# Kernel tuning notes

Hardware: AMD Instinct MI355X
Metric: run time of the kernel (lower is better)

Reference implementation:

```python
import jax, jax.numpy as jnp
import numpy as np

SEQ, IN, H = 8192, 1024, 2048

def setup_inputs() -> dict:
    key = jax.random.key(0)
    ks = jax.random.split(key, 7)
    s = 0.02
    return {
        "input_seq": jax.random.normal(ks[0], (SEQ, IN), jnp.float32),
        "W_ih": jax.random.normal(ks[1], (4 * H, IN), jnp.float32) * s,
        "W_hh": jax.random.normal(ks[2], (4 * H, H), jnp.float32) * s,
        "b_ih": jax.random.normal(ks[3], (4 * H,), jnp.float32) * s,
        "b_hh": jax.random.normal(ks[4], (4 * H,), jnpp if False else jnp.float32) * s if False else jax.random.normal(ks[4], (4 * H,), jnp.float32) * s,
        "W_lin": jax.random.normal(ks[5], (1, H), jnp.float32) * s,
        "b_lin": jax.random.normal(ks[6], (1,), jnp.float32) * s,
    }

def _lstm(input_seq, W_ih, W_hh, b, H):
    # Precompute input projections for all timesteps: [S, 4H]
    x_proj = input_seq @ W_ih.T + b

    def step(carry, xp):
        h, c = carry
        gates = xp + h @ W_hh.T  # [4H], PyTorch order: i, f, g, o
        i = jax.nn.sigmoid(gates[0:H])
        f = jax.nn.sigmoid(gates[H:2 * H])
        g = jnp.tanh(gates[2 * H:3 * H])
        o = jax.nn.sigmoid(gates[3 * H:4 * H])
        c = f * c + i * g
        h = o * jnp.tanh(c)
        return (h, c), h

    h0 = jnp.zeros((H,), input_seq.dtype)
    c0 = jnp.zeros((H,), input_seq.dtype)
    _, hs = jax.lax.scan(step, (h0, c0), x_proj)
    return hs  # [S, H]

def reference(input_seq, W_ih, W_hh, b_ih, b_hh, W_lin, b_lin):
    H_ = W_hh.shape[1]
    hs = _lstm(input_seq, W_ih, W_hh, b_ih + b_hh, H_)
    # dropout is identity in eval mode; then linear + sigmoid + flatten
    out = jax.nn.sigmoid(hs @ W_lin.T + b_lin)  # [S, 1]
    return out.reshape(-1)
```

## Files before the change

### kernel.cpp

```cpp
#include <hip/hip_runtime.h>
#include <hip/hip_bf16.h>
#include <stdint.h>

constexpr int kSEQ = 8192;
constexpr int kIN  = 1024;
constexpr int kH   = 2048;
constexpr int kG4  = 4 * kH;
constexpr int kNB  = 256;
constexpr int kHB  = kH / kNB;
constexpr int kWP  = kH + 16;

constexpr size_t OFF_HBUF  = 0;
constexpr size_t OFF_ABORT = 32768;
constexpr size_t OFF_HS    = 65536;
constexpr size_t OFF_XP    = OFF_HS + (size_t)kSEQ * kH * 2;

typedef unsigned int uint4v __attribute__((ext_vector_type(4)));
typedef __attribute__((ext_vector_type(8))) short bf16x8;
typedef __attribute__((ext_vector_type(4))) float f32x4;

__device__ __forceinline__ float bflo(uint32_t v) { return __uint_as_float(v << 16); }
__device__ __forceinline__ float bfhi(uint32_t v) { return __uint_as_float(v & 0xffff0000u); }

__global__ __launch_bounds__(256) void k_xproj(const float* __restrict__ A,
                                               const float* __restrict__ B,
                                               const float* __restrict__ bih,
                                               const float* __restrict__ bhh,
                                               __hip_bfloat16* __restrict__ C)
{
    constexpr int LDR = 40;
    __shared__ __hip_bfloat16 Al[128 * LDR];
    __shared__ __hip_bfloat16 Bl[128 * LDR];

    const int tid = threadIdx.x;
    const int bx  = blockIdx.x & 63;
    const int by  = blockIdx.x >> 6;
    const int m0  = by * 128, n0 = bx * 128;
    const int w   = tid >> 6;
    const int l   = tid & 63;
    const int wm  = w >> 1, wn = w & 1;
    const int fr  = l & 15, fg = l >> 4;

    f32x4 acc[4][4] = {};

    const int sr = tid >> 1;
    const int sh = (tid & 1) << 4;

    for (int k0 = 0; k0 < kIN; k0 += 32) {
        const float* as = A + (size_t)(m0 + sr) * kIN + k0 + sh;
        const float* bs = B + (size_t)(n0 + sr) * kIN + k0 + sh;
        float4 a0 = *(const float4*)(as);
        float4 a1 = *(const float4*)(as + 4);
        float4 a2 = *(const float4*)(as + 8);
        float4 a3 = *(const float4*)(as + 12);
        float4 b0 = *(const float4*)(bs);
        float4 b1 = *(const float4*)(bs + 4);
        float4 b2 = *(const float4*)(bs + 8);
        float4 b3 = *(const float4*)(bs + 12);
        __syncthreads();
        {
            __hip_bfloat16* ad = Al + sr * LDR + sh;
            __hip_bfloat16* bd = Bl + sr * LDR + sh;
            ad[0]=__float2bfloat16(a0.x);  ad[1]=__float2bfloat16(a0.y);
            ad[2]=__float2bfloat16(a0.z);  ad[3]=__float2bfloat16(a0.w);
            ad[4]=__float2bfloat16(a1.x);  ad[5]=__float2bfloat16(a1.y);
            ad[6]=__float2bfloat16(a1.z);  ad[7]=__float2bfloat16(a1.w);
            ad[8]=__float2bfloat16(a2.x);  ad[9]=__float2bfloat16(a2.y);
            ad[10]=__float2bfloat16(a2.z); ad[11]=__float2bfloat16(a2.w);
            ad[12]=__float2bfloat16(a3.x); ad[13]=__float2bfloat16(a3.y);
            ad[14]=__float2bfloat16(a3.z); ad[15]=__float2bfloat16(a3.w);
            bd[0]=__float2bfloat16(b0.x);  bd[1]=__float2bfloat16(b0.y);
            bd[2]=__float2bfloat16(b0.z);  bd[3]=__float2bfloat16(b0.w);
            bd[4]=__float2bfloat16(b1.x);  bd[5]=__float2bfloat16(b1.y);
            bd[6]=__float2bfloat16(b1.z);  bd[7]=__float2bfloat16(b1.w);
            bd[8]=__float2bfloat16(b2.x);  bd[9]=__float2bfloat16(b2.y);
            bd[10]=__float2bfloat16(b2.z); bd[11]=__float2bfloat16(b2.w);
            bd[12]=__float2bfloat16(b3.x); bd[13]=__float2bfloat16(b3.y);
            bd[14]=__float2bfloat16(b3.z); bd[15]=__float2bfloat16(b3.w);
        }
        __syncthreads();

        bf16x8 am[4], bn[4];
        #pragma unroll
        for (int f = 0; f < 4; ++f) {
            am[f] = *(const bf16x8*)(Al + (wm * 64 + f * 16 + fr) * LDR + fg * 8);
            bn[f] = *(const bf16x8*)(Bl + (wn * 64 + f * 16 + fr) * LDR + fg * 8);
        }
        #pragma unroll
        for (int fm = 0; fm < 4; ++fm)
            #pragma unroll
            for (int fn = 0; fn < 4; ++fn)
                acc[fm][fn] = __builtin_amdgcn_mfma_f32_16x16x32_bf16(
                                  am[fm], bn[fn], acc[fm][fn], 0, 0, 0);
    }

    #pragma unroll
    for (int fn = 0; fn < 4; ++fn) {
        const int cn = n0 + wn * 64 + fn * 16 + fr;
        const float bb = bih[cn] + bhh[cn];
        #pragma unroll
        for (int fm = 0; fm < 4; ++fm) {
            const int rbase = m0 + wm * 64 + fm * 16 + fg * 4;
            #pragma unroll
            for (int r = 0; r < 4; ++r)
                C[(size_t)(rbase + r) * kG4 + cn] = __float2bfloat16(acc[fm][fn][r] + bb);
        }
    }
}

__global__ __launch_bounds__(256, 1) void k_lstm(const float* __restrict__ Whh,
                                                 const __hip_bfloat16* __restrict__ xp,
                                                 unsigned long long* __restrict__ hbuf,
                                                 uint32_t* __restrict__ abortf,
                                                 __hip_bfloat16* __restrict__ hs)
{
    extern __shared__ char smem[];
    __hip_bfloat16* Wl  = (__hip_bfloat16*)smem;
    float*          hl2 = (float*)(smem + 32 * kWP * 2);

    const int wg  = blockIdx.x;
    const int tid = threadIdx.x;
    const int w   = tid >> 6;
    const int l   = tid & 63;
    const int hb  = wg * kHB;

    {
        const int lr = tid >> 3;
        const int g  = lr & 3;
        const int jl = 2 * (lr >> 3) + ((lr >> 2) & 1);
        const int cb = (tid & 7) * 256;
        const float* src = Whh + (size_t)(g * kH + hb + jl) * kH + cb;
        __hip_bfloat16* dst = Wl + (size_t)lr * kWP + cb;
        for (int c = 0; c < 256; c += 4) {
            float4 v = *(const float4*)(src + c);
            dst[c + 0] = __float2bfloat16(v.x);
            dst[c + 1] = __float2bfloat16(v.y);
            dst[c + 2] = __float2bfloat16(v.z);
            dst[c + 3] = __float2bfloat16(v.w);
        }
    }
    __syncthreads();

    const __hip_bfloat16* wrow = Wl + (size_t)(w * 8 + (l >> 3)) * kWP;
    const int kbase = (l & 7) * 8;
    const int jg = hb + 2 * w + (l >> 5);
    float c_state = 0.0f;
    uint32_t budget = 0;

    for (int t = 0; t < kSEQ; ++t) {
        const __hip_bfloat16* xr = xp + (size_t)t * kG4 + jg;
        const float xi = __bfloat162float(xr[0]);
        const float xf = __bfloat162float(xr[kH]);
        const float xg = __bfloat162float(xr[2 * kH]);
        const float xo = __bfloat162float(xr[3 * kH]);

        float* hw = hl2 + (size_t)(t & 1) * kH + tid * 8;
        int dead = 0;
        if (t == 0) {
            #pragma unroll
            for (int j = 0; j < 8; ++j) hw[j] = 0.f;
        } else {
            const unsigned long long* src = hbuf + (size_t)((t - 1) & 1) * kH + tid * 8;
            const uint32_t tag = (uint32_t)t;
            uint4v q0, q1, q2, q3;
            for (;;) {
                asm volatile(
                    "global_load_dwordx4 %0, %4, off sc0 sc1\n\t"
                    "global_load_dwordx4 %1, %4, off offset:16 sc0 sc1\n\t"
                    "global_load_dwordx4 %2, %4, off offset:32 sc0 sc1\n\t"
                    "global_load_dwordx4 %3, %4, off offset:48 sc0 sc1\n\t"
                    "s_waitcnt vmcnt(0)"
                    : "=&v"(q0), "=&v"(q1), "=&v"(q2), "=&v"(q3)
                    : "v"(src)
                    : "memory");
                bool ok = (q0[0] == tag) & (q0[2] == tag) & (q1[0] == tag) & (q1[2] == tag)
                        & (q2[0] == tag) & (q2[2] == tag) & (q3[0] == tag) & (q3[2] == tag);
                if (ok) break;
                if ((++budget & 15) == 0) {
                    if (__hip_atomic_load(abortf, __ATOMIC_RELAXED,
                                          __HIP_MEMORY_SCOPE_AGENT) != 0u) { dead = 1; break; }
                    if (budget > (1u << 21)) { dead = 1; break; }
                }
            }
            hw[0] = __uint_as_float(q0[1]); hw[1] = __uint_as_float(q0[3]);
            hw[2] = __uint_as_float(q1[1]); hw[3] = __uint_as_float(q1[3]);
            hw[4] = __uint_as_float(q2[1]); hw[5] = __uint_as_float(q2[3]);
            hw[6] = __uint_as_float(q3[1]); hw[7] = __uint_as_float(q3[3]);
        }
        if (__syncthreads_or(dead)) {
            __hip_atomic_store(abortf, 1u, __ATOMIC_RELAXED, __HIP_MEMORY_SCOPE_AGENT);
            return;
        }

        const float* hv = hl2 + (size_t)(t & 1) * kH;
        float acc = 0.f;
        #pragma unroll 8
        for (int it = 0; it < 32; ++it) {
            const int k = it * 64 + kbase;
            uint4 wv = *(const uint4*)(wrow + k);
            float4 h0 = *(const float4*)(hv + k);
            float4 h1 = *(const float4*)(hv + k + 4);
            acc += bflo(wv.x) * h0.x + bfhi(wv.x) * h0.y
                 + bflo(wv.y) * h0.z + bfhi(wv.y) * h0.w
                 + bflo(wv.z) * h1.x + bfhi(wv.z) * h1.y
                 + bflo(wv.w) * h1.z + bfhi(wv.w) * h1.w;
        }
        acc += __shfl_xor(acc, 1);
        acc += __shfl_xor(acc, 2);
        acc += __shfl_xor(acc, 4);

        const int base = l & 32;
        const float gi = __shfl(acc, base + 0)  + xi;
        const float gf = __shfl(acc, base + 8)  + xf;
        const float gg = __shfl(acc, base + 16) + xg;
        const float go = __shfl(acc, base + 24) + xo;
        const float si = 1.f / (1.f + expf(-gi));
        const float sf = 1.f / (1.f + expf(-gf));
        const float tg = tanhf(gg);
        const float so = 1.f / (1.f + expf(-go));
        c_state = sf * c_state + si * tg;
        const float hvv = so * tanhf(c_state);
        if ((l & 31) == 0) {
            hs[(size_t)t * kH + jg] = __float2bfloat16(hvv);
            const unsigned long long pv =
                ((unsigned long long)__float_as_uint(hvv) << 32) | (uint32_t)(t + 1);
            __hip_atomic_store(hbuf + (size_t)(t & 1) * kH + jg, pv,
                               __ATOMIC_RELAXED, __HIP_MEMORY_SCOPE_AGENT);
        }
    }
}

__global__ __launch_bounds__(256) void k_out(const __hip_bfloat16* __restrict__ hs,
                                             const float* __restrict__ wlin,
                                             const float* __restrict__ blin,
                                             float* __restrict__ out)
{
    const int w = threadIdx.x >> 6, l = threadIdx.x & 63;
    const int t = blockIdx.x * 4 + w;
    const __hip_bfloat16* row = hs + (size_t)t * kH;
    float acc = 0.f;
    #pragma unroll
    for (int i = 0; i < 4; ++i) {
        const int k = i * 512 + l * 8;
        uint4 hv = *(const uint4*)(row + k);
        float4 w0 = *(const float4*)(wlin + k);
        float4 w1 = *(const float4*)(wlin + k + 4);
        acc += bflo(hv.x) * w0.x + bfhi(hv.x) * w0.y
             + bflo(hv.y) * w0.z + bfhi(hv.y) * w0.w
             + bflo(hv.z) * w1.x + bfhi(hv.z) * w1.y
             + bflo(hv.w) * w1.z + bfhi(hv.w) * w1.w;
    }
    #pragma unroll
    for (int s = 32; s >= 1; s >>= 1) acc += __shfl_xor(acc, s);
    if (l == 0) out[t] = 1.f / (1.f + expf(-(acc + blin[0])));
}

extern "C" void kernel_launch(void* const* d_in, const int* in_sizes, int n_in,
                              void* d_out, int out_size, void* d_ws, size_t ws_size,
                              hipStream_t stream)
{
    const float* input_seq = (const float*)d_in[0];
    const float* W_ih      = (const float*)d_in[1];
    const float* W_hh      = (const float*)d_in[2];
    const float* b_ih      = (const float*)d_in[3];
    const float* b_hh      = (const float*)d_in[4];
    const float* W_lin     = (const float*)d_in[5];
    const float* b_lin     = (const float*)d_in[6];
    float* out = (float*)d_out;
    char*  ws  = (char*)d_ws;

    unsigned long long* hbuf = (unsigned long long*)(ws + OFF_HBUF);
    uint32_t*           abf  = (uint32_t*)(ws + OFF_ABORT);
    __hip_bfloat16*     hs   = (__hip_bfloat16*)(ws + OFF_HS);
    __hip_bfloat16*     xpb  = (__hip_bfloat16*)(ws + OFF_XP);

    hipMemsetAsync(ws, 0, 65536, stream);

    k_xproj<<<dim3(64 * 64), dim3(256), 0, stream>>>(input_seq, W_ih, b_ih, b_hh, xpb);

    constexpr int kLds = 32 * kWP * 2 + 2 * kH * 4;
    hipFuncSetAttribute((const void*)k_lstm, hipFuncAttributeMaxDynamicSharedMemorySize, kLds);

    {
        const float* a0 = W_hh; const __hip_bfloat16* a1 = xpb;
        unsigned long long* a2 = hbuf; uint32_t* a3 = abf; __hip_bfloat16* a4 = hs;
        void* args[5] = { &a0, &a1, &a2, &a3, &a4 };
        hipError_t ce = hipLaunchCooperativeKernel((const void*)k_lstm, dim3(kNB), dim3(256),
                                                   args, (unsigned)kLds, stream);
        if (ce != hipSuccess) {
            k_lstm<<<dim3(kNB), dim3(256), kLds, stream>>>(W_hh, xpb, hbuf, abf, hs);
        }
    }

    k_out<<<dim3(kSEQ / 4), dim3(256), 0, stream>>>(hs, W_lin, b_lin, out);
}
```

Measured before the change: 50.47 ms.

## Double LSTM recurrence block size to 512 threads, one hidden unit per wave

Raises the persistent recurrent kernel to 512 threads per block, giving 8 waves that each own one hidden unit, with 16 lanes per gate row. Each thread now polls and loads half as many tagged h values per step and runs half as many dot-product iterations. This targets shorter per-step latency on the serial recurrence critical path. The cost is an extra shuffle stage in the reduction and a larger block barrier per timestep.

```diff
diff --git a/kernel.cpp b/kernel.cpp
--- a/kernel.cpp
+++ b/kernel.cpp
@@ -108,7 +108,7 @@
     }
 }
 
-__global__ __launch_bounds__(256, 1) void k_lstm(const float* __restrict__ Whh,
+__global__ __launch_bounds__(512, 1) void k_lstm(const float* __restrict__ Whh,
                                                  const __hip_bfloat16* __restrict__ xp,
                                                  unsigned long long* __restrict__ hbuf,
                                                  uint32_t* __restrict__ abortf,
@@ -125,13 +125,13 @@
     const int hb  = wg * kHB;
 
     {
-        const int lr = tid >> 3;
+        const int lr = tid >> 4;
         const int g  = lr & 3;
-        const int jl = 2 * (lr >> 3) + ((lr >> 2) & 1);
-        const int cb = (tid & 7) * 256;
+        const int jl = lr >> 2;
+        const int cb = (tid & 15) * 128;
         const float* src = Whh + (size_t)(g * kH + hb + jl) * kH + cb;
         __hip_bfloat16* dst = Wl + (size_t)lr * kWP + cb;
-        for (int c = 0; c < 256; c += 4) {
+        for (int c = 0; c < 128; c += 4) {
             float4 v = *(const float4*)(src + c);
             dst[c + 0] = __float2bfloat16(v.x);
             dst[c + 1] = __float2bfloat16(v.y);
@@ -141,9 +141,9 @@
     }
     __syncthreads();
 
-    const __hip_bfloat16* wrow = Wl + (size_t)(w * 8 + (l >> 3)) * kWP;
-    const int kbase = (l & 7) * 8;
-    const int jg = hb + 2 * w + (l >> 5);
+    const __hip_bfloat16* wrow = Wl + (size_t)(w * 4 + (l >> 4)) * kWP;
+    const int kbase = (l & 15) * 8;
+    const int jg = hb + w;
     float c_state = 0.0f;
     uint32_t budget = 0;
 
@@ -154,27 +154,23 @@
         const float xg = __bfloat162float(xr[2 * kH]);
         const float xo = __bfloat162float(xr[3 * kH]);
 
-        float* hw = hl2 + (size_t)(t & 1) * kH + tid * 8;
+        float* hw = hl2 + (size_t)(t & 1) * kH + tid * 4;
         int dead = 0;
         if (t == 0) {
-            #pragma unroll
-            for (int j = 0; j < 8; ++j) hw[j] = 0.f;
+            hw[0] = 0.f; hw[1] = 0.f; hw[2] = 0.f; hw[3] = 0.f;
         } else {
-            const unsigned long long* src = hbuf + (size_t)((t - 1) & 1) * kH + tid * 8;
+            const unsigned long long* src = hbuf + (size_t)((t - 1) & 1) * kH + tid * 4;
             const uint32_t tag = (uint32_t)t;
-            uint4v q0, q1, q2, q3;
+            uint4v q0, q1;
             for (;;) {
                 asm volatile(
-                    "global_load_dwordx4 %0, %4, off sc0 sc1\n\t"
-                    "global_load_dwordx4 %1, %4, off offset:16 sc0 sc1\n\t"
-                    "global_load_dwordx4 %2, %4, off offset:32 sc0 sc1\n\t"
-                    "global_load_dwordx4 %3, %4, off offset:48 sc0 sc1\n\t"
+                    "global_load_dwordx4 %0, %2, off sc0 sc1\n\t"
+                    "global_load_dwordx4 %1, %2, off offset:16 sc0 sc1\n\t"
                     "s_waitcnt vmcnt(0)"
-                    : "=&v"(q0), "=&v"(q1), "=&v"(q2), "=&v"(q3)
+                    : "=&v"(q0), "=&v"(q1)
                     : "v"(src)
                     : "memory");
-                bool ok = (q0[0] == tag) & (q0[2] == tag) & (q1[0] == tag) & (q1[2] == tag)
-                        & (q2[0] == tag) & (q2[2] == tag) & (q3[0] == tag) & (q3[2] == tag);
+                bool ok = (q0[0] == tag) & (q0[2] == tag) & (q1[0] == tag) & (q1[2] == tag);
                 if (ok) break;
                 if ((++budget & 15) == 0) {
                     if (__hip_atomic_load(abortf, __ATOMIC_RELAXED,
@@ -184,8 +180,6 @@
             }
             hw[0] = __uint_as_float(q0[1]); hw[1] = __uint_as_float(q0[3]);
             hw[2] = __uint_as_float(q1[1]); hw[3] = __uint_as_float(q1[3]);
-            hw[4] = __uint_as_float(q2[1]); hw[5] = __uint_as_float(q2[3]);
-            hw[6] = __uint_as_float(q3[1]); hw[7] = __uint_as_float(q3[3]);
         }
         if (__syncthreads_or(dead)) {
             __hip_atomic_store(abortf, 1u, __ATOMIC_RELAXED, __HIP_MEMORY_SCOPE_AGENT);
@@ -195,8 +189,8 @@
         const float* hv = hl2 + (size_t)(t & 1) * kH;
         float acc = 0.f;
         #pragma unroll 8
-        for (int it = 0; it < 32; ++it) {
-            const int k = it * 64 + kbase;
+        for (int it = 0; it < 16; ++it) {
+            const int k = it * 128 + kbase;
             uint4 wv = *(const uint4*)(wrow + k);
             float4 h0 = *(const float4*)(hv + k);
             float4 h1 = *(const float4*)(hv + k + 4);
@@ -208,19 +202,19 @@
         acc += __shfl_xor(acc, 1);
         acc += __shfl_xor(acc, 2);
         acc += __shfl_xor(acc, 4);
-
-        const int base = l & 32;
-        const float gi = __shfl(acc, base + 0)  + xi;
-        const float gf = __shfl(acc, base + 8)  + xf;
-        const float gg = __shfl(acc, base + 16) + xg;
-        const float go = __shfl(acc, base + 24) + xo;
+        acc += __shfl_xor(acc, 8);
+
+        const float gi = __shfl(acc, 0)  + xi;
+        const float gf = __shfl(acc, 16) + xf;
+        const float gg = __shfl(acc, 32) + xg;
+        const float go = __shfl(acc, 48) + xo;
         const float si = 1.f / (1.f + expf(-gi));
         const float sf = 1.f / (1.f + expf(-gf));
         const float tg = tanhf(gg);
         const float so = 1.f / (1.f + expf(-go));
         c_state = sf * c_state + si * tg;
         const float hvv = so * tanhf(c_state);
-        if ((l & 31) == 0) {
+        if (l == 0) {
             hs[(size_t)t * kH + jg] = __float2bfloat16(hvv);
             const unsigned long long pv =
                 ((unsigned long long)__float_as_uint(hvv) << 32) | (uint32_t)(t + 1);
@@ -285,10 +279,10 @@
         const float* a0 = W_hh; const __hip_bfloat16* a1 = xpb;
         unsigned long long* a2 = hbuf; uint32_t* a3 = abf; __hip_bfloat16* a4 = hs;
         void* args[5] = { &a0, &a1, &a2, &a3, &a4 };
-        hipError_t ce = hipLaunchCooperativeKernel((const void*)k_lstm, dim3(kNB), dim3(256),
+        hipError_t ce = hipLaunchCooperativeKernel((const void*)k_lstm, dim3(kNB), dim3(512),
                                                    args, (unsigned)kLds, stream);
         if (ce != hipSuccess) {
-            k_lstm<<<dim3(kNB), dim3(256), kLds, stream>>>(W_hh, xpb, hbuf, abf, hs);
+            k_lstm<<<dim3(kNB), dim3(512), kLds, stream>>>(W_hh, xpb, hbuf, abf, hs);
         }
     }
 
```

Result: slower. 61.18 ms (+21.2%).
